# Kernel optimization log

Hardware: AMD Instinct MI355X
Metric: run time of the kernel (lower is better)

Reference implementation:

```python
import jax, jax.numpy as jnp
import numpy as np

N_ATOMS = 10000
N_EDGES = 160000
C_EMB = 32          # embedding_size
N_RBF = 32          # radial_features
Z_MAX = 119
CUTOFF = 5.0


def setup_inputs() -> dict:
    key = jax.random.key(0)
    ks = jax.random.split(key, 8)
    atomic_numbers = jax.random.randint(ks[0], (N_ATOMS,), 0, Z_MAX)
    neighbour_index = jax.random.randint(ks[1], (2, N_EDGES), 0, N_ATOMS)
    edge_vectors = jax.random.normal(ks[2], (N_EDGES, 3), dtype=jnp.float32) * 2.0
    z_table = jax.random.normal(ks[3], (Z_MAX, C_EMB), dtype=jnp.float32) * 0.1
    z_map_W = jax.random.normal(ks[4], (C_EMB, 2 * C_EMB), dtype=jnp.float32) * 0.1
    dense_W = jax.random.normal(ks[5], (3 * C_EMB, N_RBF), dtype=jnp.float32) * 0.1
    dense_b = jax.random.normal(ks[6], (3 * C_EMB,), dtype=jnp.float32) * 0.1
    # PhysNet-style exponential RBF parameters (graph-pes ExponentialRBF)
    c_inf = float(np.exp(-CUTOFF))
    rbf_centres = jnp.linspace(c_inf, 1.0, N_RBF, dtype=jnp.float32)
    beta_val = (2.0 / N_RBF * (1.0 - c_inf)) ** -2
    rbf_beta = jnp.full((N_RBF,), beta_val, dtype=jnp.float32)
    return {
        'atomic_numbers': atomic_numbers,
        'neighbour_index': neighbour_index,
        'edge_vectors': edge_vectors,
        'z_table': z_table,
        'z_map_W': z_map_W,
        'dense_W': dense_W,
        'dense_b': dense_b,
        'rbf_beta': rbf_beta,
        'rbf_centres': rbf_centres,
    }


def reference(atomic_numbers, neighbour_index, edge_vectors, z_table,
              z_map_W, dense_W, dense_b, rbf_beta, rbf_centres):
    # --- geometry -----------------------------------------------------
    r = jnp.linalg.norm(edge_vectors, axis=-1)              # [E]
    r_hat = edge_vectors / r[:, None]                       # [E,3]
    vx, vy, vz = r_hat[:, 0], r_hat[:, 1], r_hat[:, 2]
    zero = jnp.zeros_like(vx)
    # skew-symmetric A_0 (matches torch stack ordering)
    A0 = jnp.stack([zero, -vz, vy,
                    vz, zero, -vx,
                    -vy, vx, zero], axis=1).reshape(-1, 3, 3)   # [E,3,3]
    eye = jnp.eye(3, dtype=edge_vectors.dtype)
    outer = r_hat[:, :, None] * r_hat[:, None, :]            # [E,3,3]
    trace_mean = jnp.trace(outer, axis1=-2, axis2=-1) / 3.0  # [E]
    S0 = 0.5 * (outer + jnp.swapaxes(outer, -1, -2)) - trace_mean[:, None, None] * eye
    # --- species embedding ---------------------------------------------
    h_atom = z_table[atomic_numbers]                         # [N,C]
    h_i = h_atom[neighbour_index[0]]                         # [E,C]
    h_j = h_atom[neighbour_index[1]]                         # [E,C]
    h_z = jnp.concatenate([h_i, h_j], axis=-1) @ z_map_W.T   # [E,C]
    # --- radial embedding (exp RBF -> Linear, x cosine envelope) -------
    rbf = jnp.exp(-rbf_beta[None, :] *
                  (jnp.exp(-r)[:, None] - rbf_centres[None, :]) ** 2)  # [E,R]
    h_r = rbf @ dense_W.T + dense_b                          # [E,3C]
    env = jnp.where(r < CUTOFF,
                    0.5 * (jnp.cos(jnp.pi * r / CUTOFF) + 1.0), 0.0)
    h_r = h_r * env[:, None]
    # --- combine --------------------------------------------------------
    c = h_r * jnp.tile(h_z, (1, 3))                          # [E,3C]
    C = h_z.shape[-1]
    c_I, c_A, c_S = c[:, :C], c[:, C:2 * C], c[:, 2 * C:]
    X_I = c_I[:, :, None, None] * eye                        # [E,C,3,3]
    X_A = c_A[:, :, None, None] * A0[:, None, :, :]          # [E,C,3,3]
    X_S = c_S[:, :, None, None] * S0[:, None, :, :]          # [E,C,3,3]
    return X_I, X_A, X_S
```

## Files before the change

### kernel.cpp

```cpp
#include <hip/hip_runtime.h>

#define N_EDGES 160000
#define C_EMB 32
#define N_RBF 32
#define EPB 8
#define THREADS 256

typedef float floatx4 __attribute__((ext_vector_type(4)));

__global__ __launch_bounds__(THREADS) void edge_embed_kernel(
    const int* __restrict__ atomic_numbers,
    const int* __restrict__ nbr,
    const float* __restrict__ ev,
    const float* __restrict__ z_table,
    const float* __restrict__ z_map_W,
    const float* __restrict__ dense_W,
    const float* __restrict__ dense_b,
    const float* __restrict__ rbf_beta,
    const float* __restrict__ rbf_centres,
    float* __restrict__ out)
{
    __shared__ float s_hi[EPB][C_EMB];
    __shared__ float s_hj[EPB][C_EMB];
    __shared__ float s_rbf[EPB][N_RBF];
    __shared__ float s_hz[EPB][C_EMB];
    __shared__ float s_c[EPB][96];
    __shared__ float s_basis[EPB][28];

    const int tid = threadIdx.x;
    const int e0 = blockIdx.x * EPB;

    {
        int idx = tid;
        int e = idx >> 5, k = idx & 31;
        int ge = e0 + e;
        int zi = atomic_numbers[nbr[ge]];
        int zj = atomic_numbers[nbr[N_EDGES + ge]];
        s_hi[e][k] = z_table[zi * C_EMB + k];
        s_hj[e][k] = z_table[zj * C_EMB + k];
    }

    {
        int idx = tid;
        int e = idx >> 5, n = idx & 31;
        int ge = e0 + e;
        float x = ev[ge * 3 + 0], y = ev[ge * 3 + 1], z = ev[ge * 3 + 2];
        float r = sqrtf(x * x + y * y + z * z);
        float er = __expf(-r);
        float d = er - rbf_centres[n];
        s_rbf[e][n] = __expf(-rbf_beta[n] * d * d);
        if (n == 0) {
            s_basis[e][27] = (r < 5.0f)
                ? 0.5f * (__cosf(3.14159265358979323f * r * 0.2f) + 1.0f)
                : 0.0f;
        }
    }

    if (tid < EPB * 27) {
        int e = tid / 27, t = tid - e * 27;
        int ge = e0 + e;
        float x = ev[ge * 3 + 0], y = ev[ge * 3 + 1], z = ev[ge * 3 + 2];
        float rinv = rsqrtf(x * x + y * y + z * z);
        float vx = x * rinv, vy = y * rinv, vz = z * rinv;
        float val;
        if (t < 9) {
            val = (t == 0 || t == 4 || t == 8) ? 1.0f : 0.0f;
        } else if (t < 18) {
            int p = t - 9;
            switch (p) {
                case 1: val = -vz; break;
                case 2: val =  vy; break;
                case 3: val =  vz; break;
                case 5: val = -vx; break;
                case 6: val = -vy; break;
                case 7: val =  vx; break;
                default: val = 0.0f; break;
            }
        } else {
            int p = t - 18;
            int i = p / 3, j = p - 3 * i;
            float ri = (i == 0) ? vx : ((i == 1) ? vy : vz);
            float rj = (j == 0) ? vx : ((j == 1) ? vy : vz);
            val = ri * rj - ((i == j) ? (1.0f / 3.0f) : 0.0f);
        }
        s_basis[e][t] = val;
    }
    __syncthreads();

    {
        int idx = tid;
        int e = idx >> 5, cc = idx & 31;
        const float4* Wi  = (const float4*)(z_map_W + cc * 64);
        const float4* hi4 = (const float4*)s_hi[e];
        const float4* hj4 = (const float4*)s_hj[e];
        float acc = 0.0f;
        #pragma unroll
        for (int k = 0; k < 8; ++k) {
            float4 w = Wi[k]; float4 h = hi4[k];
            acc += w.x * h.x + w.y * h.y + w.z * h.z + w.w * h.w;
        }
        #pragma unroll
        for (int k = 0; k < 8; ++k) {
            float4 w = Wi[8 + k]; float4 h = hj4[k];
            acc += w.x * h.x + w.y * h.y + w.z * h.z + w.w * h.w;
        }
        s_hz[e][cc] = acc;
    }
    __syncthreads();

    for (int idx = tid; idx < EPB * 96; idx += THREADS) {
        int e = idx / 96, m = idx - e * 96;
        int cc = m & 31;
        const float4* Wd  = (const float4*)(dense_W + m * 32);
        const float4* rb4 = (const float4*)s_rbf[e];
        float acc = dense_b[m];
        #pragma unroll
        for (int n = 0; n < 8; ++n) {
            float4 w = Wd[n]; float4 rv = rb4[n];
            acc += w.x * rv.x + w.y * rv.y + w.z * rv.z + w.w * rv.w;
        }
        s_c[e][m] = acc * s_basis[e][27] * s_hz[e][cc];
    }
    __syncthreads();

    float* outI = out + (size_t)e0 * 288;
    float* outA = out + (size_t)N_EDGES * 288 + (size_t)e0 * 288;
    float* outS = out + (size_t)N_EDGES * 576 + (size_t)e0 * 288;
    const int NQ = EPB * 288 / 4;
    for (int q = tid; q < NQ; q += THREADS) {
        int fbase = q * 4;
        floatx4 aI, aA, aS;
        #pragma unroll
        for (int u = 0; u < 4; ++u) {
            int f = fbase + u;
            int e = f / 288;
            int rem = f - e * 288;
            int cc = rem / 9;
            int p = rem - cc * 9;
            aI[u] = s_c[e][cc]      * s_basis[e][p];
            aA[u] = s_c[e][32 + cc] * s_basis[e][9 + p];
            aS[u] = s_c[e][64 + cc] * s_basis[e][18 + p];
        }
        __builtin_nontemporal_store(aI, (floatx4*)outI + q);
        __builtin_nontemporal_store(aA, (floatx4*)outA + q);
        __builtin_nontemporal_store(aS, (floatx4*)outS + q);
    }
}

extern "C" void kernel_launch(void* const* d_in, const int* in_sizes, int n_in,
                              void* d_out, int out_size, void* d_ws, size_t ws_size,
                              hipStream_t stream) {
    const int*   an  = (const int*)d_in[0];
    const int*   nbr = (const int*)d_in[1];
    const float* ev  = (const float*)d_in[2];
    const float* zt  = (const float*)d_in[3];
    const float* zw  = (const float*)d_in[4];
    const float* dw  = (const float*)d_in[5];
    const float* db  = (const float*)d_in[6];
    const float* rb  = (const float*)d_in[7];
    const float* rc  = (const float*)d_in[8];
    float* outp = (float*)d_out;

    dim3 grid(N_EDGES / EPB);
    edge_embed_kernel<<<grid, THREADS, 0, stream>>>(
        an, nbr, ev, zt, zw, dw, db, rb, rc, outp);
}
```

Before: 376.0 us.

## Split edge embedding into feature kernel and workspace-backed expansion kernel

Splits the single fused kernel into two. The first computes per-edge coefficients and basis values into a workspace buffer. The second expands them into the three output tensors, with each block writing one contiguous output component. The aim is to make the dominant output-write phase a simple streaming kernel with more edges per block and contiguous stores, at the cost of an extra launch and a workspace round trip of about 80 MB. A fallback fused kernel with 16 edges per block and plain stores instead of nontemporal ones is kept for when the workspace is too small.

```diff
diff --git a/kernel.cpp b/kernel.cpp
--- a/kernel.cpp
+++ b/kernel.cpp
@@ -3,12 +3,15 @@
 #define N_EDGES 160000
 #define C_EMB 32
 #define N_RBF 32
-#define EPB 8
-#define THREADS 256
 
 typedef float floatx4 __attribute__((ext_vector_type(4)));
 
-__global__ __launch_bounds__(THREADS) void edge_embed_kernel(
+#define PI_F 3.14159265358979323f
+
+#define EPB1 32
+#define T1 256
+
+__global__ __launch_bounds__(T1) void k1_features(
     const int* __restrict__ atomic_numbers,
     const int* __restrict__ nbr,
     const float* __restrict__ ev,
@@ -18,47 +21,37 @@
     const float* __restrict__ dense_b,
     const float* __restrict__ rbf_beta,
     const float* __restrict__ rbf_centres,
-    float* __restrict__ out)
+    float* __restrict__ ws_c,
+    float* __restrict__ ws_basis)
 {
-    __shared__ float s_hi[EPB][C_EMB];
-    __shared__ float s_hj[EPB][C_EMB];
-    __shared__ float s_rbf[EPB][N_RBF];
-    __shared__ float s_hz[EPB][C_EMB];
-    __shared__ float s_c[EPB][96];
-    __shared__ float s_basis[EPB][28];
+    __shared__ float s_hi[EPB1][C_EMB];
+    __shared__ float s_hj[EPB1][C_EMB];
+    __shared__ float s_rbf[EPB1][N_RBF];
+    __shared__ float s_hz[EPB1][C_EMB];
+    __shared__ float s_env[EPB1];
 
     const int tid = threadIdx.x;
-    const int e0 = blockIdx.x * EPB;
-
-    {
-        int idx = tid;
-        int e = idx >> 5, k = idx & 31;
-        int ge = e0 + e;
-        int zi = atomic_numbers[nbr[ge]];
-        int zj = atomic_numbers[nbr[N_EDGES + ge]];
-        s_hi[e][k] = z_table[zi * C_EMB + k];
-        s_hj[e][k] = z_table[zj * C_EMB + k];
-    }
-
-    {
-        int idx = tid;
-        int e = idx >> 5, n = idx & 31;
-        int ge = e0 + e;
+    const int e0 = blockIdx.x * EPB1;
+
+    for (int idx = tid; idx < EPB1 * C_EMB; idx += T1) {
+        int e = idx >> 5, k = idx & 31, ge = e0 + e;
+        s_hi[e][k] = z_table[atomic_numbers[nbr[ge]] * C_EMB + k];
+        s_hj[e][k] = z_table[atomic_numbers[nbr[N_EDGES + ge]] * C_EMB + k];
+    }
+    for (int idx = tid; idx < EPB1 * N_RBF; idx += T1) {
+        int e = idx >> 5, n = idx & 31, ge = e0 + e;
         float x = ev[ge * 3 + 0], y = ev[ge * 3 + 1], z = ev[ge * 3 + 2];
         float r = sqrtf(x * x + y * y + z * z);
-        float er = __expf(-r);
-        float d = er - rbf_centres[n];
+        float d = __expf(-r) - rbf_centres[n];
         s_rbf[e][n] = __expf(-rbf_beta[n] * d * d);
         if (n == 0) {
-            s_basis[e][27] = (r < 5.0f)
-                ? 0.5f * (__cosf(3.14159265358979323f * r * 0.2f) + 1.0f)
-                : 0.0f;
-        }
-    }
-
-    if (tid < EPB * 27) {
-        int e = tid / 27, t = tid - e * 27;
-        int ge = e0 + e;
+            float env = (r < 5.0f) ? 0.5f * (__cosf(PI_F * r * 0.2f) + 1.0f) : 0.0f;
+            s_env[e] = env;
+            ws_basis[ge * 28 + 27] = env;
+        }
+    }
+    for (int idx = tid; idx < EPB1 * 27; idx += T1) {
+        int e = idx / 27, t = idx - e * 27, ge = e0 + e;
         float x = ev[ge * 3 + 0], y = ev[ge * 3 + 1], z = ev[ge * 3 + 2];
         float rinv = rsqrtf(x * x + y * y + z * z);
         float vx = x * rinv, vy = y * rinv, vz = z * rinv;
@@ -83,12 +76,11 @@
             float rj = (j == 0) ? vx : ((j == 1) ? vy : vz);
             val = ri * rj - ((i == j) ? (1.0f / 3.0f) : 0.0f);
         }
-        s_basis[e][t] = val;
-    }
-    __syncthreads();
-
-    {
-        int idx = tid;
+        ws_basis[ge * 28 + t] = val;
+    }
+    __syncthreads();
+
+    for (int idx = tid; idx < EPB1 * C_EMB; idx += T1) {
         int e = idx >> 5, cc = idx & 31;
         const float4* Wi  = (const float4*)(z_map_W + cc * 64);
         const float4* hi4 = (const float4*)s_hi[e];
@@ -108,7 +100,155 @@
     }
     __syncthreads();
 
-    for (int idx = tid; idx < EPB * 96; idx += THREADS) {
+    for (int idx = tid; idx < EPB1 * 96; idx += T1) {
+        int e = idx / 96, m = idx - e * 96, ge = e0 + e;
+        int cc = m & 31;
+        const float4* Wd  = (const float4*)(dense_W + m * 32);
+        const float4* rb4 = (const float4*)s_rbf[e];
+        float acc = dense_b[m];
+        #pragma unroll
+        for (int n = 0; n < 8; ++n) {
+            float4 w = Wd[n]; float4 rv = rb4[n];
+            acc += w.x * rv.x + w.y * rv.y + w.z * rv.z + w.w * rv.w;
+        }
+        ws_c[(size_t)ge * 96 + m] = acc * s_env[e] * s_hz[e][cc];
+    }
+}
+
+#define EPB2 32
+#define T2 256
+#define EBLK (N_EDGES / EPB2)
+
+__global__ __launch_bounds__(T2) void k2_expand(
+    const float* __restrict__ ws_c,
+    const float* __restrict__ ws_basis,
+    float* __restrict__ out)
+{
+    __shared__ float s_cc[EPB2][C_EMB];
+    __shared__ float s_bb[EPB2][12];
+
+    const int tid = threadIdx.x;
+    const int bid = blockIdx.x;
+    const int r   = bid / EBLK;
+    const int eb  = bid - r * EBLK;
+    const int e0  = eb * EPB2;
+
+    for (int idx = tid; idx < EPB2 * C_EMB; idx += T2) {
+        int e = idx >> 5, cc = idx & 31;
+        s_cc[e][cc] = ws_c[(size_t)(e0 + e) * 96 + r * 32 + cc];
+    }
+    for (int idx = tid; idx < EPB2 * 9; idx += T2) {
+        int e = idx / 9, p = idx - e * 9;
+        s_bb[e][p] = ws_basis[(e0 + e) * 28 + 9 * r + p];
+    }
+    __syncthreads();
+
+    float* ob = out + (size_t)r * N_EDGES * 288 + (size_t)e0 * 288;
+    const int NQ = EPB2 * 288 / 4;
+    #pragma unroll 3
+    for (int q = tid; q < NQ; q += T2) {
+        int f = q * 4;
+        floatx4 v;
+        #pragma unroll
+        for (int u = 0; u < 4; ++u) {
+            int ff = f + u;
+            int e = ff / 288;
+            int rem = ff - e * 288;
+            int cc = rem / 9;
+            int p = rem - cc * 9;
+            v[u] = s_cc[e][cc] * s_bb[e][p];
+        }
+        ((floatx4*)ob)[q] = v;
+    }
+}
+
+#define EPBF 16
+#define TF 256
+
+__global__ __launch_bounds__(TF) void edge_embed_fallback(
+    const int* __restrict__ atomic_numbers,
+    const int* __restrict__ nbr,
+    const float* __restrict__ ev,
+    const float* __restrict__ z_table,
+    const float* __restrict__ z_map_W,
+    const float* __restrict__ dense_W,
+    const float* __restrict__ dense_b,
+    const float* __restrict__ rbf_beta,
+    const float* __restrict__ rbf_centres,
+    float* __restrict__ out)
+{
+    __shared__ float s_hi[EPBF][C_EMB];
+    __shared__ float s_hj[EPBF][C_EMB];
+    __shared__ float s_rbf[EPBF][N_RBF];
+    __shared__ float s_hz[EPBF][C_EMB];
+    __shared__ float s_c[EPBF][96];
+    __shared__ float s_basis[EPBF][28];
+
+    const int tid = threadIdx.x;
+    const int e0 = blockIdx.x * EPBF;
+
+    for (int idx = tid; idx < EPBF * C_EMB; idx += TF) {
+        int e = idx >> 5, k = idx & 31, ge = e0 + e;
+        s_hi[e][k] = z_table[atomic_numbers[nbr[ge]] * C_EMB + k];
+        s_hj[e][k] = z_table[atomic_numbers[nbr[N_EDGES + ge]] * C_EMB + k];
+    }
+    for (int idx = tid; idx < EPBF * N_RBF; idx += TF) {
+        int e = idx >> 5, n = idx & 31, ge = e0 + e;
+        float x = ev[ge * 3 + 0], y = ev[ge * 3 + 1], z = ev[ge * 3 + 2];
+        float r = sqrtf(x * x + y * y + z * z);
+        float d = __expf(-r) - rbf_centres[n];
+        s_rbf[e][n] = __expf(-rbf_beta[n] * d * d);
+        if (n == 0)
+            s_basis[e][27] = (r < 5.0f) ? 0.5f * (__cosf(PI_F * r * 0.2f) + 1.0f) : 0.0f;
+    }
+    for (int idx = tid; idx < EPBF * 27; idx += TF) {
+        int e = idx / 27, t = idx - e * 27, ge = e0 + e;
+        float x = ev[ge * 3 + 0], y = ev[ge * 3 + 1], z = ev[ge * 3 + 2];
+        float rinv = rsqrtf(x * x + y * y + z * z);
+        float vx = x * rinv, vy = y * rinv, vz = z * rinv;
+        float val;
+        if (t < 9) val = (t == 0 || t == 4 || t == 8) ? 1.0f : 0.0f;
+        else if (t < 18) {
+            int p = t - 9;
+            switch (p) {
+                case 1: val = -vz; break;
+                case 2: val =  vy; break;
+                case 3: val =  vz; break;
+                case 5: val = -vx; break;
+                case 6: val = -vy; break;
+                case 7: val =  vx; break;
+                default: val = 0.0f; break;
+            }
+        } else {
+            int p = t - 18;
+            int i = p / 3, j = p - 3 * i;
+            float ri = (i == 0) ? vx : ((i == 1) ? vy : vz);
+            float rj = (j == 0) ? vx : ((j == 1) ? vy : vz);
+            val = ri * rj - ((i == j) ? (1.0f / 3.0f) : 0.0f);
+        }
+        s_basis[e][t] = val;
+    }
+    __syncthreads();
+    for (int idx = tid; idx < EPBF * C_EMB; idx += TF) {
+        int e = idx >> 5, cc = idx & 31;
+        const float4* Wi  = (const float4*)(z_map_W + cc * 64);
+        const float4* hi4 = (const float4*)s_hi[e];
+        const float4* hj4 = (const float4*)s_hj[e];
+        float acc = 0.0f;
+        #pragma unroll
+        for (int k = 0; k < 8; ++k) {
+            float4 w = Wi[k]; float4 h = hi4[k];
+            acc += w.x * h.x + w.y * h.y + w.z * h.z + w.w * h.w;
+        }
+        #pragma unroll
+        for (int k = 0; k < 8; ++k) {
+            float4 w = Wi[8 + k]; float4 h = hj4[k];
+            acc += w.x * h.x + w.y * h.y + w.z * h.z + w.w * h.w;
+        }
+        s_hz[e][cc] = acc;
+    }
+    __syncthreads();
+    for (int idx = tid; idx < EPBF * 96; idx += TF) {
         int e = idx / 96, m = idx - e * 96;
         int cc = m & 31;
         const float4* Wd  = (const float4*)(dense_W + m * 32);
@@ -122,12 +262,11 @@
         s_c[e][m] = acc * s_basis[e][27] * s_hz[e][cc];
     }
     __syncthreads();
-
     float* outI = out + (size_t)e0 * 288;
     float* outA = out + (size_t)N_EDGES * 288 + (size_t)e0 * 288;
     float* outS = out + (size_t)N_EDGES * 576 + (size_t)e0 * 288;
-    const int NQ = EPB * 288 / 4;
-    for (int q = tid; q < NQ; q += THREADS) {
+    const int NQ = EPBF * 288 / 4;
+    for (int q = tid; q < NQ; q += TF) {
         int fbase = q * 4;
         floatx4 aI, aA, aS;
         #pragma unroll
@@ -141,9 +280,9 @@
             aA[u] = s_c[e][32 + cc] * s_basis[e][9 + p];
             aS[u] = s_c[e][64 + cc] * s_basis[e][18 + p];
         }
-        __builtin_nontemporal_store(aI, (floatx4*)outI + q);
-        __builtin_nontemporal_store(aA, (floatx4*)outA + q);
-        __builtin_nontemporal_store(aS, (floatx4*)outS + q);
+        ((floatx4*)outI)[q] = aI;
+        ((floatx4*)outA)[q] = aA;
+        ((floatx4*)outS)[q] = aS;
     }
 }
 
@@ -161,7 +300,17 @@
     const float* rc  = (const float*)d_in[8];
     float* outp = (float*)d_out;
 
-    dim3 grid(N_EDGES / EPB);
-    edge_embed_kernel<<<grid, THREADS, 0, stream>>>(
-        an, nbr, ev, zt, zw, dw, db, rb, rc, outp);
+    const size_t need_c = (size_t)N_EDGES * 96 * sizeof(float);
+    const size_t need_b = (size_t)N_EDGES * 28 * sizeof(float);
+
+    if (ws_size >= need_c + need_b) {
+        float* ws_c     = (float*)d_ws;
+        float* ws_basis = (float*)((char*)d_ws + need_c);
+        k1_features<<<dim3(N_EDGES / EPB1), T1, 0, stream>>>(
+            an, nbr, ev, zt, zw, dw, db, rb, rc, ws_c, ws_basis);
+        k2_expand<<<dim3(3 * EBLK), T2, 0, stream>>>(ws_c, ws_basis, outp);
+    } else {
+        edge_embed_fallback<<<dim3(N_EDGES / EPBF), TF, 0, stream>>>(
+            an, nbr, ev, zt, zw, dw, db, rb, rc, outp);
+    }
 }
```

Result: slower. 414.8 us (+10.3%).
